# Optimization experiments

Measured on AMD Instinct MI355X. Metric: run time of the kernel, lower is better.

## Reference

```python
import jax, jax.numpy as jnp
import numpy as np

B, J, K, M, D = 64, 8, 64, 32, 256
TEMP = 0.1
EPS = 1e-8  # torch CosineSimilarity eps
NUM_LABELS = 16


def setup_inputs() -> dict:
    key = jax.random.key(0)
    k1, k2, k3, k4, k5 = jax.random.split(key, 5)
    return {
        "childrens": jax.random.normal(k1, (B, J, D), jnp.float32),
        "childrens_pos": jax.random.normal(k2, (B, J, D), jnp.float32),
        "childrens_negs": jax.random.normal(k3, (B, K, M, D), jnp.float32),
        "childrens_gt_labels": jax.random.randint(k4, (B, J), 0, NUM_LABELS),
        "childrens_gt_label_negs": jax.random.randint(k5, (B, K, M), 0, NUM_LABELS),
    }


def _cos(a, b):
    # cosine similarity over last axis with torch-style eps clamping
    na = jnp.maximum(jnp.linalg.norm(a, axis=-1), EPS)
    nb = jnp.maximum(jnp.linalg.norm(b, axis=-1), EPS)
    return jnp.sum(a * b, axis=-1) / (na * nb)


def reference(childrens, childrens_pos, childrens_negs, childrens_gt_labels, childrens_gt_label_negs):
    # Faithful to the original indentation bug: only the LAST child (j = J-1)
    # of each group i contributes to the loss.
    Bn = childrens.shape[0]
    child = childrens[:, -1]                    # [B, D]
    pos = childrens_pos[:, -1]                  # [B, D]
    label = childrens_gt_labels[:, -1]          # [B]

    negs = childrens_negs.reshape(Bn, -1, childrens_negs.shape[-1])   # [B, K*M, D]
    neg_labels = childrens_gt_label_negs.reshape(Bn, -1)              # [B, K*M]

    pos_sim = _cos(child, pos) / TEMP                                 # [B]
    neg_sim = _cos(child[:, None, :], negs) / TEMP                    # [B, K*M]

    # Only negatives whose gt label equals the child's label are included;
    # excluded ones get -inf so they vanish from the CE partition function.
    mask = neg_labels == label[:, None]
    neg_sim = jnp.where(mask, neg_sim, -jnp.inf)

    logits = jnp.concatenate([pos_sim[:, None], neg_sim], axis=1)     # [B, 1+K*M]
    # CrossEntropyLoss(reduction='sum') with target class 0
    loss = jax.nn.logsumexp(logits, axis=1) - pos_sim                 # [B]
    return jnp.sum(loss) / (2 * Bn)
```

## Files before the change

### kernel.cpp

```cpp
#include <hip/hip_runtime.h>
#include <math.h>

constexpr int B = 64, J = 8, K = 64, M = 32, D = 256;
constexpr int NNEG = K * M;
constexpr float TEMP = 0.1f;
constexpr float EPS = 1e-8f;
constexpr float SHIFT = 10.0f;

constexpr int SLICES = 8;
constexpr int NEG_PER_BLOCK = NNEG / SLICES;
constexpr int NBLK = B * SLICES;

__global__ __launch_bounds__(256) void neg_partial_kernel(
    const float* __restrict__ childrens,
    const int*   __restrict__ gt_labels,
    const float* __restrict__ negs,
    const int*   __restrict__ neg_labels,
    float*       __restrict__ partials) {
  const int blk  = blockIdx.x;
  const int b    = blk / SLICES;
  const int s    = blk % SLICES;
  const int tid  = threadIdx.x;
  const int lane = tid & 63;
  const int wave = tid >> 6;

  __shared__ float child_hat[D];
  __shared__ float red[4];

  const float* child = childrens + ((size_t)b * J + (J - 1)) * D;
  float cv = child[tid];
  float ss = cv * cv;
  #pragma unroll
  for (int off = 32; off > 0; off >>= 1) ss += __shfl_down(ss, off, 64);
  if (lane == 0) red[wave] = ss;
  __syncthreads();
  const float norm2 = red[0] + red[1] + red[2] + red[3];
  const float inv_n = 1.0f / fmaxf(sqrtf(norm2), EPS);
  child_hat[tid] = cv * inv_n;
  __syncthreads();

  const int label = gt_labels[b * J + (J - 1)];

  const int neg_base = s * NEG_PER_BLOCK + wave * 64;
  const int*   nl      = neg_labels + (size_t)b * NNEG;
  const float* nv_base = negs + (size_t)b * NNEG * D;

  const float4 ch = ((const float4*)child_hat)[lane];

  const int nlab = nl[neg_base + lane];
  unsigned long long mask = __ballot(nlab == label);

  float acc = 0.0f;
  while (mask) {
    const int j = __ffsll((long long)mask) - 1;
    mask &= mask - 1;
    const float4* nv = (const float4*)(nv_base + (size_t)(neg_base + j) * D);
    const float4 x = nv[lane];
    float dot = ch.x * x.x + ch.y * x.y + ch.z * x.z + ch.w * x.w;
    float nn  = x.x * x.x + x.y * x.y + x.z * x.z + x.w * x.w;
    #pragma unroll
    for (int off = 32; off > 0; off >>= 1) {
      dot += __shfl_down(dot, off, 64);
      nn  += __shfl_down(nn,  off, 64);
    }
    if (lane == 0) {
      const float sim = dot / (fmaxf(sqrtf(nn), EPS) * TEMP);
      acc += expf(sim - SHIFT);
    }
  }

  __syncthreads();
  if (lane == 0) red[wave] = acc;
  __syncthreads();
  if (tid == 0) partials[blk] = red[0] + red[1] + red[2] + red[3];
}

__global__ __launch_bounds__(256) void finalize_kernel(
    const float* __restrict__ childrens,
    const float* __restrict__ childrens_pos,
    const float* __restrict__ partials,
    float*       __restrict__ out) {
  const int tid  = threadIdx.x;
  const int lane = tid & 63;
  const int wave = tid >> 6;

  float wave_loss = 0.0f;
  for (int b = wave; b < B; b += 4) {
    const float4* child = (const float4*)(childrens     + ((size_t)b * J + (J - 1)) * D);
    const float4* pos   = (const float4*)(childrens_pos + ((size_t)b * J + (J - 1)) * D);
    const float4 c = child[lane];
    const float4 p = pos[lane];
    float cc = c.x * c.x + c.y * c.y + c.z * c.z + c.w * c.w;
    float pp = p.x * p.x + p.y * p.y + p.z * p.z + p.w * p.w;
    float cp = c.x * p.x + c.y * p.y + c.z * p.z + c.w * p.w;
    #pragma unroll
    for (int off = 32; off > 0; off >>= 1) {
      cc += __shfl_down(cc, off, 64);
      pp += __shfl_down(pp, off, 64);
      cp += __shfl_down(cp, off, 64);
    }
    if (lane == 0) {
      const float pos_sim =
          cp / (fmaxf(sqrtf(cc), EPS) * fmaxf(sqrtf(pp), EPS) * TEMP);
      float acc = expf(pos_sim - SHIFT);
      #pragma unroll
      for (int s = 0; s < SLICES; ++s) acc += partials[b * SLICES + s];
      wave_loss += logf(acc) + SHIFT - pos_sim;
    }
  }

  __shared__ float red[4];
  if (lane == 0) red[wave] = wave_loss;
  __syncthreads();
  if (tid == 0) out[0] = (red[0] + red[1] + red[2] + red[3]) / (2.0f * B);
}

extern "C" void kernel_launch(void* const* d_in, const int* in_sizes, int n_in,
                              void* d_out, int out_size, void* d_ws, size_t ws_size,
                              hipStream_t stream) {
  const float* childrens      = (const float*)d_in[0];
  const float* childrens_pos  = (const float*)d_in[1];
  const float* childrens_negs = (const float*)d_in[2];
  const int*   gt_labels      = (const int*)d_in[3];
  const int*   gt_label_negs  = (const int*)d_in[4];
  float* out = (float*)d_out;

  float* partials = (float*)d_ws;

  neg_partial_kernel<<<NBLK, 256, 0, stream>>>(
      childrens, gt_labels, childrens_negs, gt_label_negs, partials);
  finalize_kernel<<<1, 256, 0, stream>>>(
      childrens, childrens_pos, partials, out);
}
```

Baseline: 198.7 us.

## Batch four masked negatives per wave iteration and move pos-sim into partial kernel

The per-wave loop over matching negatives now gathers up to four indices at a time, issues four independent row loads and runs interleaved shuffle reductions, so more memory requests are in flight and latency is hidden better. The positive-pair cosine is computed by slice-0 blocks of the main kernel using the already-normalised child, and the finalize kernel shrinks to a single 64-thread wave that only combines partials. This adds register pressure and duplicate loads on partial batches.

After: 178.0 us. -10.4%, faster.

```diff
diff --git a/kernel.cpp b/kernel.cpp
--- a/kernel.cpp
+++ b/kernel.cpp
@@ -13,10 +13,12 @@
 
 __global__ __launch_bounds__(256) void neg_partial_kernel(
     const float* __restrict__ childrens,
+    const float* __restrict__ childrens_pos,
     const int*   __restrict__ gt_labels,
     const float* __restrict__ negs,
     const int*   __restrict__ neg_labels,
-    float*       __restrict__ partials) {
+    float*       __restrict__ partials,
+    float*       __restrict__ pos_sims) {
   const int blk  = blockIdx.x;
   const int b    = blk / SLICES;
   const int s    = blk % SLICES;
@@ -26,6 +28,8 @@
 
   __shared__ float child_hat[D];
   __shared__ float red[4];
+  __shared__ float redpp[4];
+  __shared__ float redcp[4];
 
   const float* child = childrens + ((size_t)b * J + (J - 1)) * D;
   float cv = child[tid];
@@ -52,67 +56,91 @@
 
   float acc = 0.0f;
   while (mask) {
-    const int j = __ffsll((long long)mask) - 1;
+    int idx[4];
+    int cnt = 0;
+    idx[0] = __ffsll((long long)mask) - 1;
     mask &= mask - 1;
-    const float4* nv = (const float4*)(nv_base + (size_t)(neg_base + j) * D);
-    const float4 x = nv[lane];
-    float dot = ch.x * x.x + ch.y * x.y + ch.z * x.z + ch.w * x.w;
-    float nn  = x.x * x.x + x.y * x.y + x.z * x.z + x.w * x.w;
+    cnt = 1;
+    #pragma unroll
+    for (int t = 1; t < 4; ++t) {
+      if (mask) {
+        idx[t] = __ffsll((long long)mask) - 1;
+        mask &= mask - 1;
+        ++cnt;
+      } else {
+        idx[t] = idx[0];
+      }
+    }
+
+    float dot[4], nn[4];
+    #pragma unroll
+    for (int t = 0; t < 4; ++t) {
+      const float4* nv =
+          (const float4*)(nv_base + (size_t)(neg_base + idx[t]) * D);
+      const float4 x = nv[lane];
+      dot[t] = ch.x * x.x + ch.y * x.y + ch.z * x.z + ch.w * x.w;
+      nn[t]  = x.x * x.x + x.y * x.y + x.z * x.z + x.w * x.w;
+    }
     #pragma unroll
     for (int off = 32; off > 0; off >>= 1) {
-      dot += __shfl_down(dot, off, 64);
-      nn  += __shfl_down(nn,  off, 64);
+      #pragma unroll
+      for (int t = 0; t < 4; ++t) {
+        dot[t] += __shfl_down(dot[t], off, 64);
+        nn[t]  += __shfl_down(nn[t],  off, 64);
+      }
     }
     if (lane == 0) {
-      const float sim = dot / (fmaxf(sqrtf(nn), EPS) * TEMP);
-      acc += expf(sim - SHIFT);
+      #pragma unroll
+      for (int t = 0; t < 4; ++t) {
+        if (t < cnt) {
+          const float sim = dot[t] / (fmaxf(sqrtf(nn[t]), EPS) * TEMP);
+          acc += expf(sim - SHIFT);
+        }
+      }
     }
   }
 
-  __syncthreads();
-  if (lane == 0) red[wave] = acc;
-  __syncthreads();
-  if (tid == 0) partials[blk] = red[0] + red[1] + red[2] + red[3];
-}
-
-__global__ __launch_bounds__(256) void finalize_kernel(
-    const float* __restrict__ childrens,
-    const float* __restrict__ childrens_pos,
-    const float* __restrict__ partials,
-    float*       __restrict__ out) {
-  const int tid  = threadIdx.x;
-  const int lane = tid & 63;
-  const int wave = tid >> 6;
-
-  float wave_loss = 0.0f;
-  for (int b = wave; b < B; b += 4) {
-    const float4* child = (const float4*)(childrens     + ((size_t)b * J + (J - 1)) * D);
-    const float4* pos   = (const float4*)(childrens_pos + ((size_t)b * J + (J - 1)) * D);
-    const float4 c = child[lane];
-    const float4 p = pos[lane];
-    float cc = c.x * c.x + c.y * c.y + c.z * c.z + c.w * c.w;
-    float pp = p.x * p.x + p.y * p.y + p.z * p.z + p.w * p.w;
-    float cp = c.x * p.x + c.y * p.y + c.z * p.z + c.w * p.w;
+  if (s == 0) {
+    const float* pos = childrens_pos + ((size_t)b * J + (J - 1)) * D;
+    const float pv = pos[tid];
+    float pp = pv * pv;
+    float cp = child_hat[tid] * pv;
     #pragma unroll
     for (int off = 32; off > 0; off >>= 1) {
-      cc += __shfl_down(cc, off, 64);
       pp += __shfl_down(pp, off, 64);
       cp += __shfl_down(cp, off, 64);
     }
-    if (lane == 0) {
-      const float pos_sim =
-          cp / (fmaxf(sqrtf(cc), EPS) * fmaxf(sqrtf(pp), EPS) * TEMP);
-      float acc = expf(pos_sim - SHIFT);
-      #pragma unroll
-      for (int s = 0; s < SLICES; ++s) acc += partials[b * SLICES + s];
-      wave_loss += logf(acc) + SHIFT - pos_sim;
-    }
+    if (lane == 0) { redpp[wave] = pp; redcp[wave] = cp; }
   }
 
-  __shared__ float red[4];
-  if (lane == 0) red[wave] = wave_loss;
+  if (lane == 0) red[wave] = acc;
   __syncthreads();
-  if (tid == 0) out[0] = (red[0] + red[1] + red[2] + red[3]) / (2.0f * B);
+  if (tid == 0) {
+    float total = red[0] + red[1] + red[2] + red[3];
+    if (s == 0) {
+      const float ppt = redpp[0] + redpp[1] + redpp[2] + redpp[3];
+      const float cpt = redcp[0] + redcp[1] + redcp[2] + redcp[3];
+      const float pos_sim = cpt / (fmaxf(sqrtf(ppt), EPS) * TEMP);
+      pos_sims[b] = pos_sim;
+      total += expf(pos_sim - SHIFT);
+    }
+    partials[blk] = total;
+  }
+}
+
+__global__ __launch_bounds__(64) void finalize_kernel(
+    const float* __restrict__ partials,
+    const float* __restrict__ pos_sims,
+    float*       __restrict__ out) {
+  const int lane = threadIdx.x;
+  float sum = 0.0f;
+  #pragma unroll
+  for (int t = 0; t < SLICES; ++t) sum += partials[lane * SLICES + t];
+  const float ps = pos_sims[lane];
+  float loss = logf(sum) + SHIFT - ps;
+  #pragma unroll
+  for (int off = 32; off > 0; off >>= 1) loss += __shfl_down(loss, off, 64);
+  if (lane == 0) out[0] = loss / (2.0f * B);
 }
 
 extern "C" void kernel_launch(void* const* d_in, const int* in_sizes, int n_in,
@@ -126,9 +154,10 @@
   float* out = (float*)d_out;
 
   float* partials = (float*)d_ws;
+  float* pos_sims = partials + NBLK;
 
   neg_partial_kernel<<<NBLK, 256, 0, stream>>>(
-      childrens, gt_labels, childrens_negs, gt_label_negs, partials);
-  finalize_kernel<<<1, 256, 0, stream>>>(
-      childrens, childrens_pos, partials, out);
+      childrens, childrens_pos, gt_labels, childrens_negs, gt_label_negs,
+      partials, pos_sims);
+  finalize_kernel<<<1, 64, 0, stream>>>(partials, pos_sims, out);
 }
```
